# Kernel tuning notes

Measured on AMD Instinct MI355X. Metric: run time of the kernel, lower is better.

Reference implementation:

```python
import jax, jax.numpy as jnp
import numpy as np

N_NODES = 50000
N_EDGES = 800000
IN_FEAT = 128
INTER_DIM = 128
OUT_FEAT = 128
EDGE_W_DIM = 3


def setup_inputs() -> dict:
    key = jax.random.key(0)
    ks = jax.random.split(key, 8)
    h = jax.random.normal(ks[0], (N_NODES, IN_FEAT), dtype=jnp.float32)
    edge_src = jax.random.randint(ks[1], (N_EDGES,), 0, N_NODES, dtype=jnp.int32)
    edge_dst = jax.random.randint(ks[2], (N_EDGES,), 0, N_NODES, dtype=jnp.int32)
    edge_w = jax.random.normal(ks[3], (N_EDGES, EDGE_W_DIM), dtype=jnp.float32)
    # xavier-normal-ish init, gain for relu
    gain = float(np.sqrt(2.0))
    W1 = jax.random.normal(ks[4], (INTER_DIM, IN_FEAT + EDGE_W_DIM), dtype=jnp.float32)
    W1 = W1 * (gain * np.sqrt(2.0 / (INTER_DIM + IN_FEAT + EDGE_W_DIM)))
    b1 = jnp.zeros((INTER_DIM,), dtype=jnp.float32)
    W2 = jax.random.normal(ks[5], (OUT_FEAT, IN_FEAT + INTER_DIM), dtype=jnp.float32)
    W2 = W2 * (gain * np.sqrt(2.0 / (OUT_FEAT + IN_FEAT + INTER_DIM)))
    b2 = jnp.zeros((OUT_FEAT,), dtype=jnp.float32)
    return {"h": h, "edge_src": edge_src, "edge_dst": edge_dst, "edge_w": edge_w,
            "W1": W1, "b1": b1, "W2": W2, "b2": b2}


def reference(h, edge_src, edge_dst, edge_w, W1, b1, W2, b2):
    n_nodes = h.shape[0]
    # per-edge message: concat(src node feature, edge weight) -> [E, in_feat+3]
    m = jnp.concatenate([h[edge_src], edge_w], axis=1)
    # linear1 + leaky_relu (torch default negative_slope=0.01)
    tmp = m @ W1.T + b1  # [E, inter_dim]
    tmp = jnp.where(tmp >= 0, tmp, 0.01 * tmp)
    # mean over incoming edges per destination node; zero-in-degree nodes get 0
    sums = jax.ops.segment_sum(tmp, edge_dst, num_segments=n_nodes)
    counts = jax.ops.segment_sum(jnp.ones((tmp.shape[0],), dtype=tmp.dtype),
                                 edge_dst, num_segments=n_nodes)
    h_N = sums / jnp.maximum(counts, 1.0)[:, None]  # [N, inter_dim]
    # tail: concat + linear2 + relu
    h_total = jnp.concatenate([h, h_N], axis=1)  # [N, in_feat+inter_dim]
    return jax.nn.relu(h_total @ W2.T + b2)
```

## Files before the change

kernel.cpp:

```cpp
#include <hip/hip_runtime.h>
#include <hip/hip_bf16.h>

#define N_NODES 50000
#define N_EDGES 800000
#define N_TILES 3125
#define CSR_BLOCKS 782
#define PROJ_BLOCKS 782
#define BUCKET_CAP 64

typedef __attribute__((ext_vector_type(8))) short short8;
typedef __attribute__((ext_vector_type(4))) float f32x4;
typedef __attribute__((ext_vector_type(2))) float fl2;

#define OFF_G     0
#define OFF_CUR   1600000
#define OFF_HN    6400000
#define OFF_W1BP  12866384
#define OFF_BP1   12866896
#define OFF_BP2   12875088


__device__ inline unsigned bf16rne(float f) {
    unsigned u = __float_as_uint(f);
    return (u + 0x7fffu + ((u >> 16) & 1u)) >> 16;
}
__device__ inline unsigned pk2(float lo, float hi) {
    return bf16rne(lo) | (bf16rne(hi) << 16);
}
union FragU { unsigned u[4]; short8 s; uint4 v; };

template <bool HI>
__device__ inline fl2 fp8x2_dec_w(unsigned s) {
#if __has_builtin(__builtin_amdgcn_cvt_pk_f32_fp8)
    return __builtin_amdgcn_cvt_pk_f32_fp8((int)s, HI);
#else
    unsigned v = HI ? (s >> 16) : s;
    fl2 r;
    unsigned lo = v & 0xffu, h2 = (v >> 8) & 0xffu;
    unsigned blo = ((lo & 0x80u) << 24) | ((lo & 0x7fu) << 20);
    unsigned bhi = ((h2 & 0x80u) << 24) | ((h2 & 0x7fu) << 20);
    r.x = __uint_as_float(blo) * 0x1p120f;
    r.y = __uint_as_float(bhi) * 0x1p120f;
    return r;
#endif
}
__device__ inline unsigned fp8x4_enc(float a, float b, float c, float d) {
#if __has_builtin(__builtin_amdgcn_cvt_pk_fp8_f32)
    int u = __builtin_amdgcn_cvt_pk_fp8_f32(a, b, 0, false);
    u = __builtin_amdgcn_cvt_pk_fp8_f32(c, d, u, true);
    return (unsigned)u;
#else
    auto enc1 = [](float f) -> unsigned {
        unsigned u = __float_as_uint(f);
        unsigned sg = (u >> 24) & 0x80u;
        float af = fabsf(f);
        if (af < 0x1p-6f) return sg;
        if (af >= 448.f) return sg | 0x7eu;
        unsigned v = __float_as_uint(af);
        unsigned r = v + 0xFFFFFu + ((v >> 20) & 1u);
        unsigned E = r >> 23, m = (r >> 20) & 7u;
        return sg | ((E - 120u) << 3) | m;
    };
    return enc1(a) | (enc1(b) << 8) | (enc1(c) << 16) | (enc1(d) << 24);
#endif
}

__global__ __launch_bounds__(256) void repack_zero_kernel(
        const float* __restrict__ W1, const float* __restrict__ b1,
        const float* __restrict__ W2, float* __restrict__ W1bp,
        uint4* __restrict__ Bpack1, uint4* __restrict__ Bpack2,
        int* __restrict__ cursor) {
    int tid = blockIdx.x * 256 + threadIdx.x;
    if (tid < 2048) {
        int lane = tid & 63, ent = tid >> 6;
        int n = (ent & 7) * 16 + (lane & 15);
        int k0 = (ent >> 3) * 32 + ((lane >> 4) << 3);
        const float* src = W1 + n * 131 + k0;
        FragU f;
        f.u[0] = pk2(src[0], src[1]);
        f.u[1] = pk2(src[2], src[3]);
        f.u[2] = pk2(src[4], src[5]);
        f.u[3] = pk2(src[6], src[7]);
        Bpack1[ent * 64 + lane] = f.v;
    } else if (tid < 6144) {
        int t2 = tid - 2048;
        int lane = t2 & 63, ent = t2 >> 6;
        int n = (ent & 7) * 16 + (lane & 15);
        int k0 = (ent >> 3) * 32 + ((lane >> 4) << 3);
        const float* src = W2 + n * 256 + k0;
        FragU f;
        f.u[0] = pk2(src[0], src[1]);
        f.u[1] = pk2(src[2], src[3]);
        f.u[2] = pk2(src[4], src[5]);
        f.u[3] = pk2(src[6], src[7]);
        Bpack2[ent * 64 + lane] = f.v;
    }
    if (tid < 128) {
        W1bp[tid * 4 + 0] = W1[tid * 131 + 128];
        W1bp[tid * 4 + 1] = W1[tid * 131 + 129];
        W1bp[tid * 4 + 2] = W1[tid * 131 + 130];
        W1bp[tid * 4 + 3] = b1[tid];
    }
    if (tid < N_NODES) cursor[tid] = 0;
}

__global__ __launch_bounds__(256) void fused_bucket_proj(
        const int* __restrict__ esrc, const int* __restrict__ edst,
        const float* __restrict__ ew, int* __restrict__ cursor,
        uint2* __restrict__ bkt,
        const float* __restrict__ h, const uint4* __restrict__ Bpack1,
        unsigned* __restrict__ g8) {
    __shared__ float lds[64][132];
    const int role = blockIdx.x & 1;
    const int gb = blockIdx.x >> 1;

    if (role == 0) {
        const int base = gb * 1024 + threadIdx.x;
        int dst[4], src[4];
        float w0[4], w1[4], w2[4];
        bool ok[4];
        #pragma unroll
        for (int j = 0; j < 4; j++) {
            int e = base + j * 256;
            ok[j] = e < N_EDGES;
            int ce = ok[j] ? e : 0;
            dst[j] = edst[ce];
            src[j] = esrc[ce];
            w0[j] = ew[ce * 3 + 0];
            w1[j] = ew[ce * 3 + 1];
            w2[j] = ew[ce * 3 + 2];
        }
        int pos[4];
        #pragma unroll
        for (int j = 0; j < 4; j++)
            pos[j] = ok[j] ? atomicAdd(&cursor[dst[j]], 1) : BUCKET_CAP;
        #pragma unroll
        for (int j = 0; j < 4; j++) {
            if (ok[j] && pos[j] < BUCKET_CAP) {
                uint2 rec;
                rec.x = (unsigned)src[j] | (bf16rne(w0[j]) << 16);
                rec.y = bf16rne(w1[j]) | (bf16rne(w2[j]) << 16);
                bkt[(dst[j] << 6) + pos[j]] = rec;
            }
        }
        return;
    }

    const int wave = threadIdx.x >> 6;
    const int lane = threadIdx.x & 63;
    const int T = gb * 4 + wave;

    if (T < N_TILES) {
        f32x4 acc[8];
        #pragma unroll
        for (int i = 0; i < 8; i++) acc[i] = (f32x4)(0.f);

        const int row = T * 16 + (lane & 15);
        const float* hrow = h + row * 128 + ((lane >> 4) << 3);

        #pragma unroll
        for (int kt = 0; kt < 4; kt++) {
            float4 x0 = *(const float4*)(hrow + kt * 32);
            float4 x1 = *(const float4*)(hrow + kt * 32 + 4);
            FragU a;
            a.u[0] = pk2(x0.x, x0.y);
            a.u[1] = pk2(x0.z, x0.w);
            a.u[2] = pk2(x1.x, x1.y);
            a.u[3] = pk2(x1.z, x1.w);
            #pragma unroll
            for (int nt = 0; nt < 8; nt++) {
                FragU b;
                b.v = Bpack1[(kt * 8 + nt) * 64 + lane];
                acc[nt] = __builtin_amdgcn_mfma_f32_16x16x32_bf16(a.s, b.s, acc[nt], 0, 0, 0);
            }
        }
        #pragma unroll
        for (int nt = 0; nt < 8; nt++) {
            #pragma unroll
            for (int reg = 0; reg < 4; reg++) {
                int r = ((lane >> 4) << 2) + reg;
                lds[wave * 16 + r][nt * 16 + (lane & 15)] = acc[nt][reg];
            }
        }
    }
    __syncthreads();

    const int t = threadIdx.x;
    const int nodeL = t >> 2, seg = t & 3;
    const int gnode = gb * 64 + nodeL;
    if (gnode < N_NODES) {
        #pragma unroll
        for (int i = 0; i < 2; i++) {
            const float* p = &lds[nodeL][seg * 32 + i * 16];
            uint4 o;
            o.x = fp8x4_enc(p[0],  p[1],  p[2],  p[3]);
            o.y = fp8x4_enc(p[4],  p[5],  p[6],  p[7]);
            o.z = fp8x4_enc(p[8],  p[9],  p[10], p[11]);
            o.w = fp8x4_enc(p[12], p[13], p[14], p[15]);
            ((uint4*)g8)[gnode * 8 + seg * 2 + i] = o;
        }
    }
}

#define AGG_P 4
__global__ __launch_bounds__(256) void agg_kernel(const unsigned* __restrict__ g8u,
                                                  const uint2* __restrict__ bkt,
                                                  const int* __restrict__ cursor,
                                                  const float* __restrict__ W1bp,
                                                  float* __restrict__ hN) {
    const int wave = threadIdx.x >> 6;
    const int lane = threadIdx.x & 63;
    const int half = lane >> 5;
    const int c = lane & 31;
    const int v = blockIdx.x * 4 + wave;
    if (v >= N_NODES) return;

    const int degT = cursor[v];
    const int deg = (degT < BUCKET_CAP) ? degT : BUCKET_CAP;
    const int beg = v << 6;
    const int end = beg + deg;

    const float4 w0 = ((const float4*)W1bp)[4 * c + 0];
    const float4 w1 = ((const float4*)W1bp)[4 * c + 1];
    const float4 w2 = ((const float4*)W1bp)[4 * c + 2];
    const float4 w3 = ((const float4*)W1bp)[4 * c + 3];
    const fl2 cx0 = {w0.x, w1.x}, cx1 = {w2.x, w3.x};
    const fl2 cy0 = {w0.y, w1.y}, cy1 = {w2.y, w3.y};
    const fl2 cz0 = {w0.z, w1.z}, cz1 = {w2.z, w3.z};
    const fl2 cb0 = {w0.w, w1.w}, cb1 = {w2.w, w3.w};
    const fl2 kP = (fl2)(0.505f);
    const fl2 kA = (fl2)(0.495f);

    fl2 acc0 = (fl2)(0.f), acc1 = (fl2)(0.f);

    int i = beg;
    for (; i + 2 * AGG_P <= end; i += 2 * AGG_P) {
        uint2 r[AGG_P];
        #pragma unroll
        for (int u = 0; u < AGG_P; u++) r[u] = bkt[i + 2 * u + half];
        unsigned gv[AGG_P];
        #pragma unroll
        for (int u = 0; u < AGG_P; u++) gv[u] = g8u[(r[u].x & 0xffffu) * 32 + c];
        #pragma unroll
        for (int u = 0; u < AGG_P; u++) {
            fl2 ry = (fl2)(__uint_as_float(r[u].x & 0xffff0000u));
            fl2 rz = (fl2)(__uint_as_float(r[u].y << 16));
            fl2 rw = (fl2)(__uint_as_float(r[u].y & 0xffff0000u));
            fl2 t0 = fp8x2_dec_w<false>(gv[u]) + cb0;
            t0 = __builtin_elementwise_fma(cx0, ry, t0);
            t0 = __builtin_elementwise_fma(cy0, rz, t0);
            t0 = __builtin_elementwise_fma(cz0, rw, t0);
            acc0 = __builtin_elementwise_fma(kP, t0, acc0);
            acc0 = __builtin_elementwise_fma(kA, __builtin_elementwise_abs(t0), acc0);
            fl2 t1 = fp8x2_dec_w<true>(gv[u]) + cb1;
            t1 = __builtin_elementwise_fma(cx1, ry, t1);
            t1 = __builtin_elementwise_fma(cy1, rz, t1);
            t1 = __builtin_elementwise_fma(cz1, rw, t1);
            acc1 = __builtin_elementwise_fma(kP, t1, acc1);
            acc1 = __builtin_elementwise_fma(kA, __builtin_elementwise_abs(t1), acc1);
        }
    }
    for (; i + 2 <= end; i += 2) {
        uint2 r = bkt[i + half];
        unsigned gv = g8u[(r.x & 0xffffu) * 32 + c];
        fl2 ry = (fl2)(__uint_as_float(r.x & 0xffff0000u));
        fl2 rz = (fl2)(__uint_as_float(r.y << 16));
        fl2 rw = (fl2)(__uint_as_float(r.y & 0xffff0000u));
        fl2 t0 = fp8x2_dec_w<false>(gv) + cb0;
        t0 = __builtin_elementwise_fma(cx0, ry, t0);
        t0 = __builtin_elementwise_fma(cy0, rz, t0);
        t0 = __builtin_elementwise_fma(cz0, rw, t0);
        acc0 = __builtin_elementwise_fma(kP, t0, acc0);
        acc0 = __builtin_elementwise_fma(kA, __builtin_elementwise_abs(t0), acc0);
        fl2 t1 = fp8x2_dec_w<true>(gv) + cb1;
        t1 = __builtin_elementwise_fma(cx1, ry, t1);
        t1 = __builtin_elementwise_fma(cy1, rz, t1);
        t1 = __builtin_elementwise_fma(cz1, rw, t1);
        acc1 = __builtin_elementwise_fma(kP, t1, acc1);
        acc1 = __builtin_elementwise_fma(kA, __builtin_elementwise_abs(t1), acc1);
    }
    if (i < end) {
        float sc = (half == 0) ? 1.f : 0.f;
        fl2 sP = (fl2)(0.505f * sc), sA = (fl2)(0.495f * sc);
        uint2 r = bkt[i];
        unsigned gv = g8u[(r.x & 0xffffu) * 32 + c];
        fl2 ry = (fl2)(__uint_as_float(r.x & 0xffff0000u));
        fl2 rz = (fl2)(__uint_as_float(r.y << 16));
        fl2 rw = (fl2)(__uint_as_float(r.y & 0xffff0000u));
        fl2 t0 = fp8x2_dec_w<false>(gv) + cb0;
        t0 = __builtin_elementwise_fma(cx0, ry, t0);
        t0 = __builtin_elementwise_fma(cy0, rz, t0);
        t0 = __builtin_elementwise_fma(cz0, rw, t0);
        acc0 = __builtin_elementwise_fma(sP, t0, acc0);
        acc0 = __builtin_elementwise_fma(sA, __builtin_elementwise_abs(t0), acc0);
        fl2 t1 = fp8x2_dec_w<true>(gv) + cb1;
        t1 = __builtin_elementwise_fma(cx1, ry, t1);
        t1 = __builtin_elementwise_fma(cy1, rz, t1);
        t1 = __builtin_elementwise_fma(cz1, rw, t1);
        acc1 = __builtin_elementwise_fma(sP, t1, acc1);
        acc1 = __builtin_elementwise_fma(sA, __builtin_elementwise_abs(t1), acc1);
    }

    acc0.x += __shfl_xor(acc0.x, 32);
    acc0.y += __shfl_xor(acc0.y, 32);
    acc1.x += __shfl_xor(acc1.x, 32);
    acc1.y += __shfl_xor(acc1.y, 32);
    if (half == 0) {
        float inv = 1.0f / (float)((degT > 0) ? degT : 1);
        float4 o;
        o.x = acc0.x * inv;
        o.y = acc0.y * inv;
        o.z = acc1.x * inv;
        o.w = acc1.y * inv;
        ((float4*)hN)[v * 32 + c] = o;
    }
}

__global__ __launch_bounds__(256) void final_mfma(const float* __restrict__ h,
                                                  const float* __restrict__ hN,
                                                  const uint4* __restrict__ Bpack2,
                                                  const float* __restrict__ b2,
                                                  float* __restrict__ out) {
    const int wave = threadIdx.x >> 6;
    const int lane = threadIdx.x & 63;
    const int T = blockIdx.x * 4 + wave;
    if (T >= N_TILES) return;

    f32x4 acc[8];
    #pragma unroll
    for (int i = 0; i < 8; i++) acc[i] = (f32x4)(0.f);

    const int row = T * 16 + (lane & 15);
    const int koff = (lane >> 4) << 3;
    const float* hrow = h + row * 128 + koff;
    const float* nrow = hN + row * 128 + koff;

    #pragma unroll
    for (int kt = 0; kt < 8; kt++) {
        const float* src = (kt < 4) ? (hrow + kt * 32) : (nrow + (kt - 4) * 32);
        float4 x0 = *(const float4*)(src);
        float4 x1 = *(const float4*)(src + 4);
        FragU a;
        a.u[0] = pk2(x0.x, x0.y);
        a.u[1] = pk2(x0.z, x0.w);
        a.u[2] = pk2(x1.x, x1.y);
        a.u[3] = pk2(x1.z, x1.w);
        #pragma unroll
        for (int nt = 0; nt < 8; nt++) {
            FragU b;
            b.v = Bpack2[(kt * 8 + nt) * 64 + lane];
            acc[nt] = __builtin_amdgcn_mfma_f32_16x16x32_bf16(a.s, b.s, acc[nt], 0, 0, 0);
        }
    }
    #pragma unroll
    for (int nt = 0; nt < 8; nt++) {
        int ch = nt * 16 + (lane & 15);
        float bias = b2[ch];
        #pragma unroll
        for (int reg = 0; reg < 4; reg++) {
            int node = T * 16 + ((lane >> 4) << 2) + reg;
            out[node * 128 + ch] = fmaxf(acc[nt][reg] + bias, 0.f);
        }
    }
}

extern "C" void kernel_launch(void* const* d_in, const int* in_sizes, int n_in,
                              void* d_out, int out_size, void* d_ws, size_t ws_size,
                              hipStream_t stream) {
    const float* h    = (const float*)d_in[0];
    const int*   esrc = (const int*)d_in[1];
    const int*   edst = (const int*)d_in[2];
    const float* ew   = (const float*)d_in[3];
    const float* W1   = (const float*)d_in[4];
    const float* b1   = (const float*)d_in[5];
    const float* W2   = (const float*)d_in[6];
    const float* b2   = (const float*)d_in[7];
    float* out = (float*)d_out;
    float* ws  = (float*)d_ws;

    unsigned* g8  = (unsigned*)(ws + OFF_G);
    int* cursor   = (int*)(ws + OFF_CUR);
    float* hN     = ws + OFF_HN;
    float* W1bp   = ws + OFF_W1BP;
    uint4* Bpack1 = (uint4*)(ws + OFF_BP1);
    uint4* Bpack2 = (uint4*)(ws + OFF_BP2);

    uint2* bkt = (uint2*)d_out;

    repack_zero_kernel<<<196, 256, 0, stream>>>(W1, b1, W2, W1bp, Bpack1, Bpack2, cursor);

    fused_bucket_proj<<<CSR_BLOCKS + PROJ_BLOCKS, 256, 0, stream>>>(
        esrc, edst, ew, cursor, bkt, h, Bpack1, g8);

    agg_kernel<<<(N_NODES + 3) / 4, 256, 0, stream>>>(g8, bkt, cursor, W1bp, hN);

    final_mfma<<<(N_TILES + 3) / 4, 256, 0, stream>>>(h, hN, Bpack2, b2, out);
}
```

Before: 193.9 us.

## Fuse neighbor aggregation into final MFMA kernel via LDS-staged hN tile

```diff
diff --git a/kernel.cpp b/kernel.cpp
--- a/kernel.cpp
+++ b/kernel.cpp
@@ -14,7 +14,6 @@
 
 #define OFF_G     0
 #define OFF_CUR   1600000
-#define OFF_HN    6400000
 #define OFF_W1BP  12866384
 #define OFF_BP1   12866896
 #define OFF_BP2   12875088
@@ -203,127 +202,123 @@
 }
 
 #define AGG_P 4
-__global__ __launch_bounds__(256) void agg_kernel(const unsigned* __restrict__ g8u,
-                                                  const uint2* __restrict__ bkt,
-                                                  const int* __restrict__ cursor,
-                                                  const float* __restrict__ W1bp,
-                                                  float* __restrict__ hN) {
-    const int wave = threadIdx.x >> 6;
-    const int lane = threadIdx.x & 63;
-    const int half = lane >> 5;
-    const int c = lane & 31;
-    const int v = blockIdx.x * 4 + wave;
-    if (v >= N_NODES) return;
-
-    const int degT = cursor[v];
-    const int deg = (degT < BUCKET_CAP) ? degT : BUCKET_CAP;
-    const int beg = v << 6;
-    const int end = beg + deg;
-
-    const float4 w0 = ((const float4*)W1bp)[4 * c + 0];
-    const float4 w1 = ((const float4*)W1bp)[4 * c + 1];
-    const float4 w2 = ((const float4*)W1bp)[4 * c + 2];
-    const float4 w3 = ((const float4*)W1bp)[4 * c + 3];
-    const fl2 cx0 = {w0.x, w1.x}, cx1 = {w2.x, w3.x};
-    const fl2 cy0 = {w0.y, w1.y}, cy1 = {w2.y, w3.y};
-    const fl2 cz0 = {w0.z, w1.z}, cz1 = {w2.z, w3.z};
-    const fl2 cb0 = {w0.w, w1.w}, cb1 = {w2.w, w3.w};
-    const fl2 kP = (fl2)(0.505f);
-    const fl2 kA = (fl2)(0.495f);
-
-    fl2 acc0 = (fl2)(0.f), acc1 = (fl2)(0.f);
-
-    int i = beg;
-    for (; i + 2 * AGG_P <= end; i += 2 * AGG_P) {
-        uint2 r[AGG_P];
-        #pragma unroll
-        for (int u = 0; u < AGG_P; u++) r[u] = bkt[i + 2 * u + half];
-        unsigned gv[AGG_P];
-        #pragma unroll
-        for (int u = 0; u < AGG_P; u++) gv[u] = g8u[(r[u].x & 0xffffu) * 32 + c];
-        #pragma unroll
-        for (int u = 0; u < AGG_P; u++) {
-            fl2 ry = (fl2)(__uint_as_float(r[u].x & 0xffff0000u));
-            fl2 rz = (fl2)(__uint_as_float(r[u].y << 16));
-            fl2 rw = (fl2)(__uint_as_float(r[u].y & 0xffff0000u));
-            fl2 t0 = fp8x2_dec_w<false>(gv[u]) + cb0;
-            t0 = __builtin_elementwise_fma(cx0, ry, t0);
-            t0 = __builtin_elementwise_fma(cy0, rz, t0);
-            t0 = __builtin_elementwise_fma(cz0, rw, t0);
-            acc0 = __builtin_elementwise_fma(kP, t0, acc0);
-            acc0 = __builtin_elementwise_fma(kA, __builtin_elementwise_abs(t0), acc0);
-            fl2 t1 = fp8x2_dec_w<true>(gv[u]) + cb1;
-            t1 = __builtin_elementwise_fma(cx1, ry, t1);
-            t1 = __builtin_elementwise_fma(cy1, rz, t1);
-            t1 = __builtin_elementwise_fma(cz1, rw, t1);
-            acc1 = __builtin_elementwise_fma(kP, t1, acc1);
-            acc1 = __builtin_elementwise_fma(kA, __builtin_elementwise_abs(t1), acc1);
-        }
-    }
-    for (; i + 2 <= end; i += 2) {
-        uint2 r = bkt[i + half];
-        unsigned gv = g8u[(r.x & 0xffffu) * 32 + c];
-        fl2 ry = (fl2)(__uint_as_float(r.x & 0xffff0000u));
-        fl2 rz = (fl2)(__uint_as_float(r.y << 16));
-        fl2 rw = (fl2)(__uint_as_float(r.y & 0xffff0000u));
-        fl2 t0 = fp8x2_dec_w<false>(gv) + cb0;
-        t0 = __builtin_elementwise_fma(cx0, ry, t0);
-        t0 = __builtin_elementwise_fma(cy0, rz, t0);
-        t0 = __builtin_elementwise_fma(cz0, rw, t0);
-        acc0 = __builtin_elementwise_fma(kP, t0, acc0);
-        acc0 = __builtin_elementwise_fma(kA, __builtin_elementwise_abs(t0), acc0);
-        fl2 t1 = fp8x2_dec_w<true>(gv) + cb1;
-        t1 = __builtin_elementwise_fma(cx1, ry, t1);
-        t1 = __builtin_elementwise_fma(cy1, rz, t1);
-        t1 = __builtin_elementwise_fma(cz1, rw, t1);
-        acc1 = __builtin_elementwise_fma(kP, t1, acc1);
-        acc1 = __builtin_elementwise_fma(kA, __builtin_elementwise_abs(t1), acc1);
-    }
-    if (i < end) {
-        float sc = (half == 0) ? 1.f : 0.f;
-        fl2 sP = (fl2)(0.505f * sc), sA = (fl2)(0.495f * sc);
-        uint2 r = bkt[i];
-        unsigned gv = g8u[(r.x & 0xffffu) * 32 + c];
-        fl2 ry = (fl2)(__uint_as_float(r.x & 0xffff0000u));
-        fl2 rz = (fl2)(__uint_as_float(r.y << 16));
-        fl2 rw = (fl2)(__uint_as_float(r.y & 0xffff0000u));
-        fl2 t0 = fp8x2_dec_w<false>(gv) + cb0;
-        t0 = __builtin_elementwise_fma(cx0, ry, t0);
-        t0 = __builtin_elementwise_fma(cy0, rz, t0);
-        t0 = __builtin_elementwise_fma(cz0, rw, t0);
-        acc0 = __builtin_elementwise_fma(sP, t0, acc0);
-        acc0 = __builtin_elementwise_fma(sA, __builtin_elementwise_abs(t0), acc0);
-        fl2 t1 = fp8x2_dec_w<true>(gv) + cb1;
-        t1 = __builtin_elementwise_fma(cx1, ry, t1);
-        t1 = __builtin_elementwise_fma(cy1, rz, t1);
-        t1 = __builtin_elementwise_fma(cz1, rw, t1);
-        acc1 = __builtin_elementwise_fma(sP, t1, acc1);
-        acc1 = __builtin_elementwise_fma(sA, __builtin_elementwise_abs(t1), acc1);
-    }
-
-    acc0.x += __shfl_xor(acc0.x, 32);
-    acc0.y += __shfl_xor(acc0.y, 32);
-    acc1.x += __shfl_xor(acc1.x, 32);
-    acc1.y += __shfl_xor(acc1.y, 32);
-    if (half == 0) {
-        float inv = 1.0f / (float)((degT > 0) ? degT : 1);
-        float4 o;
-        o.x = acc0.x * inv;
-        o.y = acc0.y * inv;
-        o.z = acc1.x * inv;
-        o.w = acc1.y * inv;
-        ((float4*)hN)[v * 32 + c] = o;
-    }
-}
-
-__global__ __launch_bounds__(256) void final_mfma(const float* __restrict__ h,
-                                                  const float* __restrict__ hN,
-                                                  const uint4* __restrict__ Bpack2,
-                                                  const float* __restrict__ b2,
-                                                  float* __restrict__ out) {
+__global__ __launch_bounds__(256) void fused_agg_final(
+        const unsigned* __restrict__ g8u, const uint2* __restrict__ bkt,
+        const int* __restrict__ cursor, const float* __restrict__ W1bp,
+        const float* __restrict__ h, const uint4* __restrict__ Bpack2,
+        const float* __restrict__ b2, float* __restrict__ out) {
+    __shared__ float lds[64][132];
     const int wave = threadIdx.x >> 6;
     const int lane = threadIdx.x & 63;
     const int T = blockIdx.x * 4 + wave;
+
+    if (T < N_TILES) {
+        const int half = lane >> 5;
+        const int c = lane & 31;
+        const float4 w0 = ((const float4*)W1bp)[4 * c + 0];
+        const float4 w1 = ((const float4*)W1bp)[4 * c + 1];
+        const float4 w2 = ((const float4*)W1bp)[4 * c + 2];
+        const float4 w3 = ((const float4*)W1bp)[4 * c + 3];
+        const fl2 cx0 = {w0.x, w1.x}, cx1 = {w2.x, w3.x};
+        const fl2 cy0 = {w0.y, w1.y}, cy1 = {w2.y, w3.y};
+        const fl2 cz0 = {w0.z, w1.z}, cz1 = {w2.z, w3.z};
+        const fl2 cb0 = {w0.w, w1.w}, cb1 = {w2.w, w3.w};
+        const fl2 kP = (fl2)(0.505f);
+        const fl2 kA = (fl2)(0.495f);
+
+        for (int n = 0; n < 16; n++) {
+            const int v = T * 16 + n;
+            const int degT = cursor[v];
+            const int deg = (degT < BUCKET_CAP) ? degT : BUCKET_CAP;
+            const int beg = v << 6;
+            const int end = beg + deg;
+
+            fl2 acc0 = (fl2)(0.f), acc1 = (fl2)(0.f);
+            int i = beg;
+            for (; i + 2 * AGG_P <= end; i += 2 * AGG_P) {
+                uint2 r[AGG_P];
+                #pragma unroll
+                for (int u = 0; u < AGG_P; u++) r[u] = bkt[i + 2 * u + half];
+                unsigned gv[AGG_P];
+                #pragma unroll
+                for (int u = 0; u < AGG_P; u++) gv[u] = g8u[(r[u].x & 0xffffu) * 32 + c];
+                #pragma unroll
+                for (int u = 0; u < AGG_P; u++) {
+                    fl2 ry = (fl2)(__uint_as_float(r[u].x & 0xffff0000u));
+                    fl2 rz = (fl2)(__uint_as_float(r[u].y << 16));
+                    fl2 rw = (fl2)(__uint_as_float(r[u].y & 0xffff0000u));
+                    fl2 t0 = fp8x2_dec_w<false>(gv[u]) + cb0;
+                    t0 = __builtin_elementwise_fma(cx0, ry, t0);
+                    t0 = __builtin_elementwise_fma(cy0, rz, t0);
+                    t0 = __builtin_elementwise_fma(cz0, rw, t0);
+                    acc0 = __builtin_elementwise_fma(kP, t0, acc0);
+                    acc0 = __builtin_elementwise_fma(kA, __builtin_elementwise_abs(t0), acc0);
+                    fl2 t1 = fp8x2_dec_w<true>(gv[u]) + cb1;
+                    t1 = __builtin_elementwise_fma(cx1, ry, t1);
+                    t1 = __builtin_elementwise_fma(cy1, rz, t1);
+                    t1 = __builtin_elementwise_fma(cz1, rw, t1);
+                    acc1 = __builtin_elementwise_fma(kP, t1, acc1);
+                    acc1 = __builtin_elementwise_fma(kA, __builtin_elementwise_abs(t1), acc1);
+                }
+            }
+            for (; i + 2 <= end; i += 2) {
+                uint2 r = bkt[i + half];
+                unsigned gv = g8u[(r.x & 0xffffu) * 32 + c];
+                fl2 ry = (fl2)(__uint_as_float(r.x & 0xffff0000u));
+                fl2 rz = (fl2)(__uint_as_float(r.y << 16));
+                fl2 rw = (fl2)(__uint_as_float(r.y & 0xffff0000u));
+                fl2 t0 = fp8x2_dec_w<false>(gv) + cb0;
+                t0 = __builtin_elementwise_fma(cx0, ry, t0);
+                t0 = __builtin_elementwise_fma(cy0, rz, t0);
+                t0 = __builtin_elementwise_fma(cz0, rw, t0);
+                acc0 = __builtin_elementwise_fma(kP, t0, acc0);
+                acc0 = __builtin_elementwise_fma(kA, __builtin_elementwise_abs(t0), acc0);
+                fl2 t1 = fp8x2_dec_w<true>(gv) + cb1;
+                t1 = __builtin_elementwise_fma(cx1, ry, t1);
+                t1 = __builtin_elementwise_fma(cy1, rz, t1);
+                t1 = __builtin_elementwise_fma(cz1, rw, t1);
+                acc1 = __builtin_elementwise_fma(kP, t1, acc1);
+                acc1 = __builtin_elementwise_fma(kA, __builtin_elementwise_abs(t1), acc1);
+            }
+            if (i < end) {
+                float sc = (half == 0) ? 1.f : 0.f;
+                fl2 sP = (fl2)(0.505f * sc), sA = (fl2)(0.495f * sc);
+                uint2 r = bkt[i];
+                unsigned gv = g8u[(r.x & 0xffffu) * 32 + c];
+                fl2 ry = (fl2)(__uint_as_float(r.x & 0xffff0000u));
+                fl2 rz = (fl2)(__uint_as_float(r.y << 16));
+                fl2 rw = (fl2)(__uint_as_float(r.y & 0xffff0000u));
+                fl2 t0 = fp8x2_dec_w<false>(gv) + cb0;
+                t0 = __builtin_elementwise_fma(cx0, ry, t0);
+                t0 = __builtin_elementwise_fma(cy0, rz, t0);
+                t0 = __builtin_elementwise_fma(cz0, rw, t0);
+                acc0 = __builtin_elementwise_fma(sP, t0, acc0);
+                acc0 = __builtin_elementwise_fma(sA, __builtin_elementwise_abs(t0), acc0);
+                fl2 t1 = fp8x2_dec_w<true>(gv) + cb1;
+                t1 = __builtin_elementwise_fma(cx1, ry, t1);
+                t1 = __builtin_elementwise_fma(cy1, rz, t1);
+                t1 = __builtin_elementwise_fma(cz1, rw, t1);
+                acc1 = __builtin_elementwise_fma(sP, t1, acc1);
+                acc1 = __builtin_elementwise_fma(sA, __builtin_elementwise_abs(t1), acc1);
+            }
+
+            acc0.x += __shfl_xor(acc0.x, 32);
+            acc0.y += __shfl_xor(acc0.y, 32);
+            acc1.x += __shfl_xor(acc1.x, 32);
+            acc1.y += __shfl_xor(acc1.y, 32);
+            if (half == 0) {
+                float inv = 1.0f / (float)((degT > 0) ? degT : 1);
+                float4 o;
+                o.x = acc0.x * inv;
+                o.y = acc0.y * inv;
+                o.z = acc1.x * inv;
+                o.w = acc1.y * inv;
+                *(float4*)&lds[wave * 16 + n][4 * c] = o;
+            }
+        }
+    }
+    __syncthreads();
+
     if (T >= N_TILES) return;
 
     f32x4 acc[8];
@@ -333,7 +328,7 @@
     const int row = T * 16 + (lane & 15);
     const int koff = (lane >> 4) << 3;
     const float* hrow = h + row * 128 + koff;
-    const float* nrow = hN + row * 128 + koff;
+    const float* nrow = &lds[wave * 16 + (lane & 15)][koff];
 
     #pragma unroll
     for (int kt = 0; kt < 8; kt++) {
@@ -380,7 +375,6 @@
 
     unsigned* g8  = (unsigned*)(ws + OFF_G);
     int* cursor   = (int*)(ws + OFF_CUR);
-    float* hN     = ws + OFF_HN;
     float* W1bp   = ws + OFF_W1BP;
     uint4* Bpack1 = (uint4*)(ws + OFF_BP1);
     uint4* Bpack2 = (uint4*)(ws + OFF_BP2);
@@ -392,7 +386,6 @@
     fused_bucket_proj<<<CSR_BLOCKS + PROJ_BLOCKS, 256, 0, stream>>>(
         esrc, edst, ew, cursor, bkt, h, Bpack1, g8);
 
-    agg_kernel<<<(N_NODES + 3) / 4, 256, 0, stream>>>(g8, bkt, cursor, W1bp, hN);
-
-    final_mfma<<<(N_TILES + 3) / 4, 256, 0, stream>>>(h, hN, Bpack2, b2, out);
-}
+    fused_agg_final<<<(N_TILES + 3) / 4, 256, 0, stream>>>(
+        g8, bkt, cursor, W1bp, h, Bpack2, b2, out);
+}
```

After: 200.1 us. 3.2% more time.
